# Performance work log

Measured on AMD Instinct MI355X. Metric: run time of the kernel, lower is better.

The kernel has to match this reference:

```python
import jax, jax.numpy as jnp
import numpy as np

EPS = 1e-7        # keras backend epsilon
ALPHA = 0.25
GAMMA = 2.0
NEG_INF = -1e30

B, T, V, L = 256, 1024, 128, 64
BLANK = V - 1     # blank_index=-1 in tf ctc_loss_v2


def setup_inputs() -> dict:
    key = jax.random.key(0)
    k1, k2 = jax.random.split(key)
    y_pred = jax.random.uniform(k1, (B, T, V), dtype=jnp.float32)
    y_true = jax.random.randint(k2, (B, L), 0, V - 1, dtype=jnp.int32)
    return {"y_true": y_true, "y_pred": y_pred}


def _ctc_neg_log_lik(y_true, y_pred):
    """Standard CTC forward (alpha) DP in log space; full lengths T and L."""
    b, t, v = y_pred.shape
    l = y_true.shape[1]
    s = 2 * l + 1
    # tf ctc_loss_v2 log-softmaxes its logits; logits here are log(y_pred+eps)
    logp = jax.nn.log_softmax(jnp.log(y_pred + EPS), axis=-1)     # [B,T,V]
    # extended label sequence: blank, l1, blank, l2, ..., blank    [B,S]
    ext = jnp.full((b, s), BLANK, dtype=y_true.dtype)
    ext = ext.at[:, 1::2].set(y_true)
    # per-timestep log-probs of extended labels -> [T,B,S]
    lp_ext = jnp.take_along_axis(logp, ext[:, None, :], axis=2)   # [B,T,S]
    lp_ext = jnp.transpose(lp_ext, (1, 0, 2))                     # [T,B,S]
    # skip transition s-2 -> s allowed iff ext[s] != blank and ext[s] != ext[s-2]
    ext_sm2 = jnp.pad(ext[:, :-2], ((0, 0), (2, 0)), constant_values=BLANK)
    allow_skip = (ext != BLANK) & (ext != ext_sm2)                # [B,S]

    alpha0 = jnp.full((b, s), NEG_INF, dtype=logp.dtype)
    alpha0 = alpha0.at[:, 0].set(lp_ext[0, :, 0])
    alpha0 = alpha0.at[:, 1].set(lp_ext[0, :, 1])

    def step(alpha, lp_t):
        a0 = alpha
        a1 = jnp.pad(alpha[:, :-1], ((0, 0), (1, 0)), constant_values=NEG_INF)
        a2 = jnp.pad(alpha[:, :-2], ((0, 0), (2, 0)), constant_values=NEG_INF)
        a2 = jnp.where(allow_skip, a2, NEG_INF)
        m = jnp.maximum(jnp.maximum(a0, a1), a2)                  # stable LSE
        lse = m + jnp.log(jnp.exp(a0 - m) + jnp.exp(a1 - m) + jnp.exp(a2 - m))
        return lse + lp_t, None

    alphaT, _ = jax.lax.scan(step, alpha0, lp_ext[1:])
    log_lik = jnp.logaddexp(alphaT[:, -1], alphaT[:, -2])         # [B]
    return -log_lik


def reference(y_true, y_pred):
    loss = _ctc_neg_log_lik(y_true, y_pred)                       # [B]
    p = jnp.exp(-loss)
    focal = ALPHA * (1.0 - p) ** GAMMA * loss
    return jnp.mean(focal)
```

## Files before the change

kernel.cpp:

```cpp
#include <hip/hip_runtime.h>


#define EPSF 1e-7f

constexpr int Bb  = 256;
constexpr int Tt  = 1024;
constexpr int Vv  = 128;
constexpr int Ll  = 64;
constexpr int CH  = 64;
constexpr int NCH = Tt / CH;
constexpr int NPH = NCH + 1;
constexpr int NSH = 26;

template <int Ctrl, int RowMask, int BankMask, bool BoundCtrl>
__device__ __forceinline__ float dppf(float x) {
    return __int_as_float(__builtin_amdgcn_update_dpp(
        0, __float_as_int(x), Ctrl, RowMask, BankMask, BoundCtrl));
}

__device__ __forceinline__ float wave_sum63(float x) {
    x += dppf<0x111, 0xf, 0xf, true>(x);
    x += dppf<0x112, 0xf, 0xf, true>(x);
    x += dppf<0x114, 0xf, 0xf, true>(x);
    x += dppf<0x118, 0xf, 0xf, true>(x);
    x += dppf<0x142, 0xa, 0xf, false>(x);
    x += dppf<0x143, 0xc, 0xf, false>(x);
    return x;
}

__device__ __forceinline__ float half_sum(float x) {
    x += dppf<0x111, 0xf, 0xf, true>(x);
    x += dppf<0x112, 0xf, 0xf, true>(x);
    x += dppf<0x114, 0xf, 0xf, true>(x);
    x += dppf<0x118, 0xf, 0xf, true>(x);
    x += dppf<0x142, 0xa, 0xf, false>(x);
    return x;
}

__device__ __forceinline__ float wave_max63(float x) {
    x = fmaxf(x, dppf<0x111, 0xf, 0xf, true>(x));
    x = fmaxf(x, dppf<0x112, 0xf, 0xf, true>(x));
    x = fmaxf(x, dppf<0x114, 0xf, 0xf, true>(x));
    x = fmaxf(x, dppf<0x118, 0xf, 0xf, true>(x));
    x = fmaxf(x, dppf<0x142, 0xa, 0xf, false>(x));
    x = fmaxf(x, dppf<0x143, 0xc, 0xf, false>(x));
    return x;
}

__device__ __forceinline__ float bcast63(float x) {
    return __int_as_float(__builtin_amdgcn_readlane(__float_as_int(x), 63));
}

#define DO_STEP(QE, QB, CHK)                                                 \
    do {                                                                     \
        const float am1_ = dppf<0x138, 0xf, 0xf, true>(a_odd);               \
        const float ne_  = (a_even + am1_) * (QB);                           \
        const float no_  = fmaf(maskf, am1_, a_odd + a_even) * (QE);         \
        const float n1_  = (a128 + a_odd) * (QB);                            \
        a_even = ne_; a_odd = no_; a128 = n1_;                               \
        if (CHK) {                                                           \
            const float m_ = fmaxf(fmaxf(a_even, a_odd), a128);              \
            if (__all(m_ < 0x1p-75f)) {                                      \
                const float    wmax_  = bcast63(wave_max63(m_));             \
                const unsigned e_     = __float_as_uint(wmax_) >> 23;        \
                const float    scale_ = __uint_as_float((254u - e_) << 23);  \
                eacc += (int)e_ - 127;                                       \
                a_even *= scale_; a_odd *= scale_; a128 *= scale_;           \
            }                                                                \
        }                                                                    \
    } while (0)

__launch_bounds__(1024, 1)
__global__ void fused_kernel(const int* __restrict__ y_true,
                             const float* __restrict__ y_pred,
                             float* __restrict__ focal_ws) {
    const int b    = blockIdx.x;
    const int lane = threadIdx.x & 63;
    const int wv   = threadIdx.x >> 6;

    const float*  ygl = y_pred + (size_t)b * Tt * Vv;
    const float4* yb4 = (const float4*)ygl;

    __shared__ float4 gt4[2 * (CH / 4) * 64];
    __shared__ float4 bk4[2 * (CH / 4)];
    __shared__ float  part[NSH];

    int lab = 0;
    if (wv <= 2) lab = y_true[b * Ll + lane];

    float a_even = 0.0f, a_odd = 0.0f, a128 = 0.0f, maskf = 0.0f;
    int   eacc = 0;
    if (wv == 0) {
        const int labp = __shfl_up(lab, 1);
        maskf  = (lane == 0 || lab != labp) ? 1.0f : 0.0f;
        a_even = (lane == 0) ? 1.0f : 0.0f;
    }

    const int h   = 2 * (wv - 3) + (lane >> 5);
    const int c32 = lane & 31;
    float ll = 0.0f;

    for (int p = 0; p < NPH; ++p) {
        if (wv >= 3) {
            if (p < NCH) {
                const float4* src4 = yb4 + p * CH * (Vv / 4);
                const float4 v0 = src4[h * 32 + c32];
                const float4 v1 = src4[(h + 26) * 32 + c32];
                const float  s0 = half_sum(v0.x + v0.y + v0.z + v0.w);
                const float  s1 = half_sum(v1.x + v1.y + v1.z + v1.w);
                if (c32 == 31)
                    ll += __log2f(s0 + (float)Vv * EPSF) +
                          __log2f(s1 + (float)Vv * EPSF);
                if (h < 12) {
                    const float4 v2 = src4[(h + 52) * 32 + c32];
                    const float  s2 = half_sum(v2.x + v2.y + v2.z + v2.w);
                    if (c32 == 31) ll += __log2f(s2 + (float)Vv * EPSF);
                }
            } else if (c32 == 31) {
                part[h] = ll;
            }
        } else if (wv >= 1) {
            if (p < NCH) {
                const int    tg0 = (wv - 1) * 32;
                const float* src = ygl + p * CH * Vv;
                float* gtw = (float*)(gt4 + (p & 1) * (CH / 4) * 64);
#pragma unroll 8
                for (int j = 0; j < 32; ++j) {
                    const int tl = tg0 + j;
                    gtw[(tl >> 2) * 256 + lane * 4 + (tl & 3)] =
                        src[tl * Vv + lab];
                }
                if (lane < 32) {
                    const int tl = tg0 + lane;
                    ((float*)(bk4 + (p & 1) * (CH / 4)))[tl] =
                        src[tl * Vv + (Vv - 1)];
                }
            }
        } else {
            const int c = p - 1;
            if (c >= 0) {
                __builtin_amdgcn_s_setprio(1);
                const float4* gbf = gt4 + (c & 1) * (CH / 4) * 64;
                const float4* bbf = bk4 + (c & 1) * (CH / 4);
                float4 gA = gbf[0 * 64 + lane], gB = gbf[1 * 64 + lane];
                float4 bA = bbf[0],             bB = bbf[1];
#pragma unroll
                for (int i = 0; i < 16; ++i) {
                    DO_STEP(gA.x + EPSF, bA.x + EPSF, false);
                    DO_STEP(gA.y + EPSF, bA.y + EPSF, false);
                    DO_STEP(gA.z + EPSF, bA.z + EPSF, false);
                    DO_STEP(gA.w + EPSF, bA.w + EPSF, (i & 3) == 3);
                    gA = gB; bA = bB;
                    if (i < 14) {
                        gB = gbf[(i + 2) * 64 + lane];
                        bB = bbf[i + 2];
                    }
                }
                __builtin_amdgcn_s_setprio(0);
            }
        }
        __syncthreads();
    }

    if (wv == 0) {
        float vs = (lane < NSH) ? part[lane] : 0.0f;
        vs = wave_sum63(vs);
        if (lane == 63) {
            const float acc_ld  = vs;
            const float tot     = fmaxf(a128 + a_odd, 1e-37f);
            const float log2lik = __log2f(tot) + (float)eacc - acc_ld;
            const float ln_lik  = 0.69314718055994530942f * log2lik;
            const float loss    = -ln_lik;
            const float pp      = __expf(ln_lik);
            const float om      = 1.0f - pp;
            focal_ws[b] = 0.25f * om * om * loss;
        }
    }
}

__global__ void finalize_kernel(const float* __restrict__ focal_ws,
                                float* __restrict__ out) {
    const int i    = threadIdx.x;
    const int lane = i & 63;
    const int wv   = i >> 6;

    float f = focal_ws[i];
#pragma unroll
    for (int off = 32; off > 0; off >>= 1) f += __shfl_xor(f, off);

    __shared__ float red[4];
    if (lane == 0) red[wv] = f;
    __syncthreads();
    if (i == 0)
        out[0] = (red[0] + red[1] + red[2] + red[3]) * (1.0f / (float)Bb);
}

extern "C" void kernel_launch(void* const* d_in, const int* in_sizes, int n_in,
                              void* d_out, int out_size, void* d_ws, size_t ws_size,
                              hipStream_t stream) {
    const int*   y_true = (const int*)d_in[0];
    const float* y_pred = (const float*)d_in[1];
    float* focal_ws = (float*)d_ws;

    fused_kernel<<<Bb, 1024, 0, stream>>>(y_true, y_pred, focal_ws);
    finalize_kernel<<<1, 256, 0, stream>>>(focal_ws, (float*)d_out);
}
```

Baseline: 198.5 us.

## Split softmax denominator into separate blocks and shrink CTC blocks to 256 threads

The per-timestep softmax normaliser (log of row sums) moves out of the 1024-thread CTC blocks into 2048 extra 256-thread blocks, each covering one of eight time segments of a batch row. Their partial sums go to a workspace, and the finalize kernel now combines numerator and denominator and computes the focal loss. The CTC blocks shrink to 4 waves with a 32-step chunk, so more of them can share a CU and the serial DP no longer competes with the denominator waves. In exchange, the blank column and label gathers are spread over fewer waves, the smaller chunk means twice as many barriers, and y_pred is read by two different sets of blocks.

```diff
diff --git a/kernel.cpp b/kernel.cpp
--- a/kernel.cpp
+++ b/kernel.cpp
@@ -7,25 +7,15 @@
 constexpr int Tt  = 1024;
 constexpr int Vv  = 128;
 constexpr int Ll  = 64;
-constexpr int CH  = 64;
+constexpr int CH  = 32;
 constexpr int NCH = Tt / CH;
 constexpr int NPH = NCH + 1;
-constexpr int NSH = 26;
+constexpr int NSEG = 8;
 
 template <int Ctrl, int RowMask, int BankMask, bool BoundCtrl>
 __device__ __forceinline__ float dppf(float x) {
     return __int_as_float(__builtin_amdgcn_update_dpp(
         0, __float_as_int(x), Ctrl, RowMask, BankMask, BoundCtrl));
-}
-
-__device__ __forceinline__ float wave_sum63(float x) {
-    x += dppf<0x111, 0xf, 0xf, true>(x);
-    x += dppf<0x112, 0xf, 0xf, true>(x);
-    x += dppf<0x114, 0xf, 0xf, true>(x);
-    x += dppf<0x118, 0xf, 0xf, true>(x);
-    x += dppf<0x142, 0xa, 0xf, false>(x);
-    x += dppf<0x143, 0xc, 0xf, false>(x);
-    return x;
 }
 
 __device__ __forceinline__ float half_sum(float x) {
@@ -70,23 +60,48 @@
         }                                                                    \
     } while (0)
 
-__launch_bounds__(1024, 1)
+__launch_bounds__(256)
 __global__ void fused_kernel(const int* __restrict__ y_true,
                              const float* __restrict__ y_pred,
-                             float* __restrict__ focal_ws) {
-    const int b    = blockIdx.x;
+                             float* __restrict__ num_ws,
+                             float* __restrict__ den_ws) {
     const int lane = threadIdx.x & 63;
     const int wv   = threadIdx.x >> 6;
 
-    const float*  ygl = y_pred + (size_t)b * Tt * Vv;
-    const float4* yb4 = (const float4*)ygl;
-
     __shared__ float4 gt4[2 * (CH / 4) * 64];
     __shared__ float4 bk4[2 * (CH / 4)];
-    __shared__ float  part[NSH];
-
-    int lab = 0;
-    if (wv <= 2) lab = y_true[b * Ll + lane];
+    __shared__ float  dpart[8];
+
+    if (blockIdx.x >= Bb) {
+        const int idx = blockIdx.x - Bb;
+        const int b   = idx >> 3;
+        const int seg = idx & (NSEG - 1);
+        const float4* src4 =
+            (const float4*)(y_pred + (size_t)b * Tt * Vv) +
+            seg * (Tt / NSEG) * (Vv / 4);
+        const int h   = 2 * wv + (lane >> 5);
+        const int c32 = lane & 31;
+        float ll = 0.0f;
+#pragma unroll
+        for (int k = 0; k < 16; ++k) {
+            const int r = h + 8 * k;
+            const float4 v = src4[r * 32 + c32];
+            const float  s = half_sum(v.x + v.y + v.z + v.w);
+            if (c32 == 31) ll += __log2f(s + (float)Vv * EPSF);
+        }
+        if (c32 == 31) dpart[h] = ll;
+        __syncthreads();
+        if (threadIdx.x == 0) {
+            float s = dpart[0] + dpart[1] + dpart[2] + dpart[3] +
+                      dpart[4] + dpart[5] + dpart[6] + dpart[7];
+            den_ws[seg * Bb + b] = s;
+        }
+        return;
+    }
+
+    const int    b   = blockIdx.x;
+    const float* ygl = y_pred + (size_t)b * Tt * Vv;
+    const int    lab = y_true[b * Ll + lane];
 
     float a_even = 0.0f, a_odd = 0.0f, a128 = 0.0f, maskf = 0.0f;
     int   eacc = 0;
@@ -96,44 +111,22 @@
         a_even = (lane == 0) ? 1.0f : 0.0f;
     }
 
-    const int h   = 2 * (wv - 3) + (lane >> 5);
-    const int c32 = lane & 31;
-    float ll = 0.0f;
-
     for (int p = 0; p < NPH; ++p) {
-        if (wv >= 3) {
-            if (p < NCH) {
-                const float4* src4 = yb4 + p * CH * (Vv / 4);
-                const float4 v0 = src4[h * 32 + c32];
-                const float4 v1 = src4[(h + 26) * 32 + c32];
-                const float  s0 = half_sum(v0.x + v0.y + v0.z + v0.w);
-                const float  s1 = half_sum(v1.x + v1.y + v1.z + v1.w);
-                if (c32 == 31)
-                    ll += __log2f(s0 + (float)Vv * EPSF) +
-                          __log2f(s1 + (float)Vv * EPSF);
-                if (h < 12) {
-                    const float4 v2 = src4[(h + 52) * 32 + c32];
-                    const float  s2 = half_sum(v2.x + v2.y + v2.z + v2.w);
-                    if (c32 == 31) ll += __log2f(s2 + (float)Vv * EPSF);
-                }
-            } else if (c32 == 31) {
-                part[h] = ll;
+        if (wv == 3) {
+            if (p < NCH && lane < CH) {
+                ((float*)(bk4 + (p & 1) * (CH / 4)))[lane] =
+                    ygl[(p * CH + lane) * Vv + (Vv - 1)];
             }
         } else if (wv >= 1) {
             if (p < NCH) {
-                const int    tg0 = (wv - 1) * 32;
+                const int    tg0 = (wv - 1) * (CH / 2);
                 const float* src = ygl + p * CH * Vv;
                 float* gtw = (float*)(gt4 + (p & 1) * (CH / 4) * 64);
 #pragma unroll 8
-                for (int j = 0; j < 32; ++j) {
+                for (int j = 0; j < CH / 2; ++j) {
                     const int tl = tg0 + j;
                     gtw[(tl >> 2) * 256 + lane * 4 + (tl & 3)] =
                         src[tl * Vv + lab];
-                }
-                if (lane < 32) {
-                    const int tl = tg0 + lane;
-                    ((float*)(bk4 + (p & 1) * (CH / 4)))[tl] =
-                        src[tl * Vv + (Vv - 1)];
                 }
             }
         } else {
@@ -145,13 +138,13 @@
                 float4 gA = gbf[0 * 64 + lane], gB = gbf[1 * 64 + lane];
                 float4 bA = bbf[0],             bB = bbf[1];
 #pragma unroll
-                for (int i = 0; i < 16; ++i) {
+                for (int i = 0; i < CH / 4; ++i) {
                     DO_STEP(gA.x + EPSF, bA.x + EPSF, false);
                     DO_STEP(gA.y + EPSF, bA.y + EPSF, false);
                     DO_STEP(gA.z + EPSF, bA.z + EPSF, false);
                     DO_STEP(gA.w + EPSF, bA.w + EPSF, (i & 3) == 3);
                     gA = gB; bA = bB;
-                    if (i < 14) {
+                    if (i < CH / 4 - 2) {
                         gB = gbf[(i + 2) * 64 + lane];
                         bB = bbf[i + 2];
                     }
@@ -162,29 +155,30 @@
         __syncthreads();
     }
 
-    if (wv == 0) {
-        float vs = (lane < NSH) ? part[lane] : 0.0f;
-        vs = wave_sum63(vs);
-        if (lane == 63) {
-            const float acc_ld  = vs;
-            const float tot     = fmaxf(a128 + a_odd, 1e-37f);
-            const float log2lik = __log2f(tot) + (float)eacc - acc_ld;
-            const float ln_lik  = 0.69314718055994530942f * log2lik;
-            const float loss    = -ln_lik;
-            const float pp      = __expf(ln_lik);
-            const float om      = 1.0f - pp;
-            focal_ws[b] = 0.25f * om * om * loss;
-        }
-    }
-}
-
-__global__ void finalize_kernel(const float* __restrict__ focal_ws,
+    if (wv == 0 && lane == 63) {
+        const float tot = fmaxf(a128 + a_odd, 1e-37f);
+        num_ws[b] = __log2f(tot) + (float)eacc;
+    }
+}
+
+__global__ void finalize_kernel(const float* __restrict__ num_ws,
+                                const float* __restrict__ den_ws,
                                 float* __restrict__ out) {
     const int i    = threadIdx.x;
     const int lane = i & 63;
     const int wv   = i >> 6;
 
-    float f = focal_ws[i];
+    float ds = 0.0f;
+#pragma unroll
+    for (int k = 0; k < NSEG; ++k) ds += den_ws[k * Bb + i];
+
+    const float log2lik = num_ws[i] - ds;
+    const float ln_lik  = 0.69314718055994530942f * log2lik;
+    const float loss    = -ln_lik;
+    const float pp      = __expf(ln_lik);
+    const float om      = 1.0f - pp;
+    float f = 0.25f * om * om * loss;
+
 #pragma unroll
     for (int off = 32; off > 0; off >>= 1) f += __shfl_xor(f, off);
 
@@ -200,8 +194,10 @@
                               hipStream_t stream) {
     const int*   y_true = (const int*)d_in[0];
     const float* y_pred = (const float*)d_in[1];
-    float* focal_ws = (float*)d_ws;
-
-    fused_kernel<<<Bb, 1024, 0, stream>>>(y_true, y_pred, focal_ws);
-    finalize_kernel<<<1, 256, 0, stream>>>(focal_ws, (float*)d_out);
-}
+    float* num_ws = (float*)d_ws;
+    float* den_ws = num_ws + Bb;
+
+    fused_kernel<<<Bb + Bb * NSEG, 256, 0, stream>>>(y_true, y_pred,
+                                                     num_ws, den_ws);
+    finalize_kernel<<<1, 256, 0, stream>>>(num_ws, den_ws, (float*)d_out);
+}
```

Measured after the change: 215.2 us. +8.4%, slower.
